# Kernel tuning notes

Hardware: AMD Instinct MI355X
Metric: run time of the kernel (lower is better)

The kernel has to match this reference:

```python
import jax, jax.numpy as jnp
import numpy as np

B, T, D_IN, H, D_OUT = 256, 2048, 128, 128, 128


def setup_inputs() -> dict:
    key = jax.random.key(0)
    ks = jax.random.split(key, 7)
    s_in = 1.0 / np.sqrt(H)
    return {
        "x": jax.random.normal(ks[0], (B, T, D_IN), dtype=jnp.float32),
        "Wih": jax.random.normal(ks[1], (4 * H, D_IN), dtype=jnp.float32) * s_in,
        "Whh": jax.random.normal(ks[2], (4 * H, H), dtype=jnp.float32) * s_in,
        "bih": jax.random.normal(ks[3], (4 * H,), dtype=jnp.float32) * s_in,
        "bhh": jax.random.normal(ks[4], (4 * H,), dtype=jnp.float32) * s_in,
        "Wo": jax.random.normal(ks[5], (D_OUT, H), dtype=jnp.float32) * s_in,
        "bo": jax.random.normal(ks[6], (D_OUT,), dtype=jnp.float32) * s_in,
    }


def reference(x, Wih, Whh, bih, bhh, Wo, bo):
    # LSTM recurrence over time; module returns only the last step's
    # output projection (outputs[:, -1, :]).
    batch, seq_len, _ = x.shape
    h0 = jnp.zeros((batch, Whh.shape[1]), dtype=x.dtype)
    c0 = jnp.zeros_like(h0)
    # Precompute input-side gate projections for all timesteps in one GEMM.
    xg = jnp.einsum('btd,gd->btg', x, Wih) + bih + bhh  # [B, T, 4H]
    xg = jnp.swapaxes(xg, 0, 1)  # [T, B, 4H] for scan

    def step(carry, xg_t):
        h, c = carry
        gates = xg_t + h @ Whh.T  # [B, 4H]
        i, f, g, o = jnp.split(gates, 4, axis=-1)
        i = jax.nn.sigmoid(i)
        f = jax.nn.sigmoid(f)
        g = jnp.tanh(g)
        o = jax.nn.sigmoid(o)
        c = f * c + i * g
        h = o * jnp.tanh(c)
        return (h, c), None

    (h_last, _), _ = jax.lax.scan(step, (h0, c0), xg)
    return h_last @ Wo.T + bo  # [B, D_OUT]
```

## Files before the change

kernel.cpp:

```cpp
#include <hip/hip_runtime.h>
#include <hip/hip_fp16.h>

#define B_  256
#define T_  2048
#define D_  128
#define H_  128
#define CH  32
#define NCH (T_ / CH)
#define XGP (4 * H_ + 8)

#define NLOG2E  (-1.4426950408889634f)
#define LOG2E2  ( 2.8853900817779268f)

typedef __attribute__((ext_vector_type(8))) _Float16 half8v;
typedef __attribute__((ext_vector_type(2))) _Float16 half2v;
typedef __attribute__((ext_vector_type(4))) float    floatx4;

static __device__ __forceinline__ unsigned pkh(float a, float b) {
  return __builtin_bit_cast(unsigned, __builtin_amdgcn_cvt_pkrtz(a, b));
}
static __device__ __forceinline__ float h2f_lo(unsigned u) {
  return __half2float(__ushort_as_half((unsigned short)(u & 0xffffu)));
}
static __device__ __forceinline__ float h2f_hi(unsigned u) {
  return __half2float(__ushort_as_half((unsigned short)(u >> 16)));
}
static __device__ __forceinline__ float fdot2(unsigned h, unsigned w, float c) {
  return __builtin_amdgcn_fdot2(__builtin_bit_cast(half2v, h),
                                __builtin_bit_cast(half2v, w), c, false);
}
template <int CTRL>
static __device__ __forceinline__ float dppadd(float v) {
  int t = __builtin_amdgcn_update_dpp(0, __builtin_bit_cast(int, v),
                                      CTRL, 0xF, 0xF, false);
  return v + __builtin_bit_cast(float, t);
}

__global__ __attribute__((amdgpu_flat_work_group_size(512, 512),
                          amdgpu_waves_per_eu(2, 2)))
void lstm_dot2(
    const float* __restrict__ x,   const float* __restrict__ Wih,
    const float* __restrict__ Whh, const float* __restrict__ bih,
    const float* __restrict__ bhh, const float* __restrict__ Wo,
    const float* __restrict__ bo,  float* __restrict__ out)
{
  __shared__ unsigned       xs[CH][68];
  __shared__ unsigned short xgf[CH][XGP];
  __shared__ __align__(16) unsigned hbuf[2][64];

  const int tid  = threadIdx.x;
  const int b    = blockIdx.x;
  const int lane = tid & 63;
  const int wv   = tid >> 6;
  const int quad = lane >> 4;
  const int m16  = lane & 15;
  const int unit_l = quad * 4 + (m16 & 3);
  const int unit_g = wv * 16 + unit_l;
  const int kq   = m16 >> 2;

  unsigned wd[4][16];
  #pragma unroll
  for (int g = 0; g < 4; ++g) {
    float s = (g == 2) ? LOG2E2 : NLOG2E;
    const float4* p =
        (const float4*)(Whh + (size_t)(g * 128 + unit_g) * H_) + kq * 8;
    #pragma unroll
    for (int q = 0; q < 8; ++q) {
      float4 f = p[q];
      wd[g][q * 2]     = pkh(f.x * s, f.y * s);
      wd[g][q * 2 + 1] = pkh(f.z * s, f.w * s);
    }
  }

  const float sW = ((wv >> 1) == 2) ? LOG2E2 : NLOG2E;
  uint4 wb[4][4];
  float bv[4];
  #pragma unroll
  for (int nt = 0; nt < 4; ++nt) {
    int gcol = wv * 64 + nt * 16 + m16;
    const float4* p = (const float4*)(Wih + (size_t)gcol * D_);
    #pragma unroll
    for (int kf = 0; kf < 4; ++kf) {
      float4 f0 = p[kf * 8 + quad * 2];
      float4 f1 = p[kf * 8 + quad * 2 + 1];
      uint4 u;
      u.x = pkh(f0.x * sW, f0.y * sW);  u.y = pkh(f0.z * sW, f0.w * sW);
      u.z = pkh(f1.x * sW, f1.y * sW);  u.w = pkh(f1.z * sW, f1.w * sW);
      wb[nt][kf] = u;
    }
    bv[nt] = (bih[gcol] + bhh[gcol]) * sW;
  }

  if (tid < 128) hbuf[tid >> 6][tid & 63] = 0u;
  const floatx4 zf = {0.f, 0.f, 0.f, 0.f};
  float c = 0.0f;
  __syncthreads();

  const float* xb = x + (size_t)b * T_ * D_;

  for (int ch = 0; ch < NCH; ++ch) {
    const float4* xsrc = (const float4*)(xb + (size_t)ch * CH * D_);
    #pragma unroll
    for (int i = 0; i < 2; ++i) {
      int fi = i * 512 + tid;
      float4 v = xsrc[fi];
      int t  = fi >> 5;
      int kp = (fi & 31) * 2;
      xs[t][kp]     = pkh(v.x, v.y);
      xs[t][kp + 1] = pkh(v.z, v.w);
    }
    __syncthreads();

    #pragma unroll
    for (int mt = 0; mt < 2; ++mt) {
      half8v af[4];
      #pragma unroll
      for (int kf = 0; kf < 4; ++kf)
        af[kf] = __builtin_bit_cast(half8v,
                   *(const uint4*)&xs[mt * 16 + m16][kf * 16 + quad * 4]);
      #pragma unroll
      for (int nt = 0; nt < 4; ++nt) {
        floatx4 acc = zf;
        #pragma unroll
        for (int kf = 0; kf < 4; ++kf)
          acc = __builtin_amdgcn_mfma_f32_16x16x32_f16(
              af[kf], __builtin_bit_cast(half8v, wb[nt][kf]), acc, 0, 0, 0);
        int gcol = wv * 64 + nt * 16 + m16;
        int jc   = gcol & 127, gt = gcol >> 7;
        #pragma unroll
        for (int r = 0; r < 4; ++r) {
          int trow = mt * 16 + quad * 4 + r;
          xgf[trow][jc * 4 + gt] =
              __half_as_ushort(__float2half((acc[r] + bv[nt]) * 0.25f));
        }
      }
    }
    __syncthreads();

    #pragma unroll 2
    for (int tt = 0; tt < CH; ++tt) {
      const int rp = tt & 1;
      unsigned long long xv =
          *(const unsigned long long*)&xgf[tt][unit_g * 4];
      const unsigned* hb = &hbuf[rp][kq * 16];
      unsigned hs[16];
      *(uint4*)&hs[0]  = *(const uint4*)(hb + 0);
      *(uint4*)&hs[4]  = *(const uint4*)(hb + 4);
      *(uint4*)&hs[8]  = *(const uint4*)(hb + 8);
      *(uint4*)&hs[12] = *(const uint4*)(hb + 12);
      unsigned xlo = (unsigned)xv, xhi = (unsigned)(xv >> 32);
      float ai = h2f_lo(xlo), af_ = h2f_hi(xlo);
      float ag = h2f_lo(xhi), ao  = h2f_hi(xhi);
      #pragma unroll
      for (int p = 0; p < 16; ++p) {
        ai  = fdot2(hs[p], wd[0][p], ai);
        af_ = fdot2(hs[p], wd[1][p], af_);
        ag  = fdot2(hs[p], wd[2][p], ag);
        ao  = fdot2(hs[p], wd[3][p], ao);
      }
      ai  = dppadd<0x124>(dppadd<0x128>(ai));
      af_ = dppadd<0x124>(dppadd<0x128>(af_));
      ag  = dppadd<0x124>(dppadd<0x128>(ag));
      ao  = dppadd<0x124>(dppadd<0x128>(ao));
      float gi = __builtin_amdgcn_rcpf(1.0f + __builtin_amdgcn_exp2f(ai));
      float gf = __builtin_amdgcn_rcpf(1.0f + __builtin_amdgcn_exp2f(af_));
      float go = __builtin_amdgcn_rcpf(1.0f + __builtin_amdgcn_exp2f(ao));
      float gg = 1.0f - 2.0f * __builtin_amdgcn_rcpf(
                     1.0f + __builtin_amdgcn_exp2f(ag));
      c = gf * c + gi * gg;
      float tc = 1.0f - 2.0f * __builtin_amdgcn_rcpf(
                     1.0f + __builtin_amdgcn_exp2f(c * LOG2E2));
      float h = go * tc;
      if (m16 < 4)
        ((unsigned short*)hbuf[rp ^ 1])[unit_g] =
            __half_as_ushort(__float2half(h));
      __syncthreads();
    }
  }

  if (tid < H_) {
    float acc = bo[tid];
    const float4* wr = (const float4*)(Wo + (size_t)tid * H_);
    const uint2* hp = (const uint2*)hbuf[0];
    #pragma unroll
    for (int k4 = 0; k4 < 32; ++k4) {
      float4 w  = wr[k4];
      uint2  hu = hp[k4];
      acc += w.x * h2f_lo(hu.x) + w.y * h2f_hi(hu.x)
           + w.z * h2f_lo(hu.y) + w.w * h2f_hi(hu.y);
    }
    out[(size_t)b * H_ + tid] = acc;
  }
}

extern "C" void kernel_launch(void* const* d_in, const int* in_sizes, int n_in,
                              void* d_out, int out_size, void* d_ws, size_t ws_size,
                              hipStream_t stream) {
  (void)in_sizes; (void)n_in; (void)d_ws; (void)ws_size; (void)out_size;
  const float* x   = (const float*)d_in[0];
  const float* Wih = (const float*)d_in[1];
  const float* Whh = (const float*)d_in[2];
  const float* bih = (const float*)d_in[3];
  const float* bhh = (const float*)d_in[4];
  const float* Wo  = (const float*)d_in[5];
  const float* bo  = (const float*)d_in[6];
  lstm_dot2<<<B_, 512, 0, stream>>>(x, Wih, Whh, bih, bhh, Wo, bo, (float*)d_out);
}
```

Before: 1.413 ms.

## Split recurrent gate matvec between MFMA (i,f) and fdot2 (g,o) paths

The per-timestep h·Whh product for the input and forget gates now runs on MFMA 16x16x32 instructions, with h broadcast as the B operand. The g and o gates keep the VALU fdot2 path with DPP reductions. Splitting the work this way halves the fdot2 chain on the serial critical path and uses the matrix cores in parallel with it. The cost is wasted MFMA columns, extra LDS loads of h per step, and per-lane selection of the accumulator element.

```diff
diff --git a/kernel.cpp b/kernel.cpp
--- a/kernel.cpp
+++ b/kernel.cpp
@@ -35,10 +35,12 @@
                                       CTRL, 0xF, 0xF, false);
   return v + __builtin_bit_cast(float, t);
 }
+#define SEL4(v, n) (((n) & 2) ? (((n) & 1) ? (v)[3] : (v)[2]) \
+                              : (((n) & 1) ? (v)[1] : (v)[0]))
 
 __global__ __attribute__((amdgpu_flat_work_group_size(512, 512),
                           amdgpu_waves_per_eu(2, 2)))
-void lstm_dot2(
+void lstm_hyb(
     const float* __restrict__ x,   const float* __restrict__ Wih,
     const float* __restrict__ Whh, const float* __restrict__ bih,
     const float* __restrict__ bhh, const float* __restrict__ Wo,
@@ -58,17 +60,34 @@
   const int unit_g = wv * 16 + unit_l;
   const int kq   = m16 >> 2;
 
-  unsigned wd[4][16];
+  uint4 wa[2][4];
   #pragma unroll
-  for (int g = 0; g < 4; ++g) {
-    float s = (g == 2) ? LOG2E2 : NLOG2E;
-    const float4* p =
-        (const float4*)(Whh + (size_t)(g * 128 + unit_g) * H_) + kq * 8;
+  for (int g = 0; g < 2; ++g) {
+    const float4* p = (const float4*)(Whh + (size_t)(g * 128 + wv * 16 + m16) * H_);
+    #pragma unroll
+    for (int kf = 0; kf < 4; ++kf) {
+      float4 f0 = p[kf * 8 + quad * 2];
+      float4 f1 = p[kf * 8 + quad * 2 + 1];
+      uint4 u;
+      u.x = pkh(f0.x * NLOG2E, f0.y * NLOG2E);  u.y = pkh(f0.z * NLOG2E, f0.w * NLOG2E);
+      u.z = pkh(f1.x * NLOG2E, f1.y * NLOG2E);  u.w = pkh(f1.z * NLOG2E, f1.w * NLOG2E);
+      wa[g][kf] = u;
+    }
+  }
+
+  unsigned wdg[16], wdo[16];
+  {
+    const float4* pg =
+        (const float4*)(Whh + (size_t)(2 * 128 + unit_g) * H_) + kq * 8;
+    const float4* po =
+        (const float4*)(Whh + (size_t)(3 * 128 + unit_g) * H_) + kq * 8;
     #pragma unroll
     for (int q = 0; q < 8; ++q) {
-      float4 f = p[q];
-      wd[g][q * 2]     = pkh(f.x * s, f.y * s);
-      wd[g][q * 2 + 1] = pkh(f.z * s, f.w * s);
+      float4 fg = pg[q], fo = po[q];
+      wdg[q * 2]     = pkh(fg.x * LOG2E2, fg.y * LOG2E2);
+      wdg[q * 2 + 1] = pkh(fg.z * LOG2E2, fg.w * LOG2E2);
+      wdo[q * 2]     = pkh(fo.x * NLOG2E, fo.y * NLOG2E);
+      wdo[q * 2 + 1] = pkh(fo.z * NLOG2E, fo.w * NLOG2E);
     }
   }
 
@@ -142,28 +161,50 @@
       const int rp = tt & 1;
       unsigned long long xv =
           *(const unsigned long long*)&xgf[tt][unit_g * 4];
+      uint4 hfr[4];
+      #pragma unroll
+      for (int kf = 0; kf < 4; ++kf)
+        hfr[kf] = *(const uint4*)&hbuf[rp][kf * 16 + quad * 4];
       const unsigned* hb = &hbuf[rp][kq * 16];
       unsigned hs[16];
       *(uint4*)&hs[0]  = *(const uint4*)(hb + 0);
       *(uint4*)&hs[4]  = *(const uint4*)(hb + 4);
       *(uint4*)&hs[8]  = *(const uint4*)(hb + 8);
       *(uint4*)&hs[12] = *(const uint4*)(hb + 12);
+
+      floatx4 accI, accF;
+      {
+        half8v hbv = __builtin_bit_cast(half8v, hfr[0]);
+        accI = __builtin_amdgcn_mfma_f32_16x16x32_f16(
+                   __builtin_bit_cast(half8v, wa[0][0]), hbv, zf, 0, 0, 0);
+        accF = __builtin_amdgcn_mfma_f32_16x16x32_f16(
+                   __builtin_bit_cast(half8v, wa[1][0]), hbv, zf, 0, 0, 0);
+      }
+      #pragma unroll
+      for (int kf = 1; kf < 4; ++kf) {
+        half8v hbv = __builtin_bit_cast(half8v, hfr[kf]);
+        accI = __builtin_amdgcn_mfma_f32_16x16x32_f16(
+                   __builtin_bit_cast(half8v, wa[0][kf]), hbv, accI, 0, 0, 0);
+        accF = __builtin_amdgcn_mfma_f32_16x16x32_f16(
+                   __builtin_bit_cast(half8v, wa[1][kf]), hbv, accF, 0, 0, 0);
+      }
+
       unsigned xlo = (unsigned)xv, xhi = (unsigned)(xv >> 32);
-      float ai = h2f_lo(xlo), af_ = h2f_hi(xlo);
-      float ag = h2f_lo(xhi), ao  = h2f_hi(xhi);
+      float ag = h2f_lo(xhi), ao = h2f_hi(xhi);
       #pragma unroll
       for (int p = 0; p < 16; ++p) {
-        ai  = fdot2(hs[p], wd[0][p], ai);
-        af_ = fdot2(hs[p], wd[1][p], af_);
-        ag  = fdot2(hs[p], wd[2][p], ag);
-        ao  = fdot2(hs[p], wd[3][p], ao);
-      }
-      ai  = dppadd<0x124>(dppadd<0x128>(ai));
-      af_ = dppadd<0x124>(dppadd<0x128>(af_));
-      ag  = dppadd<0x124>(dppadd<0x128>(ag));
-      ao  = dppadd<0x124>(dppadd<0x128>(ao));
-      float gi = __builtin_amdgcn_rcpf(1.0f + __builtin_amdgcn_exp2f(ai));
-      float gf = __builtin_amdgcn_rcpf(1.0f + __builtin_amdgcn_exp2f(af_));
+        ag = fdot2(hs[p], wdg[p], ag);
+        ao = fdot2(hs[p], wdo[p], ao);
+      }
+      ag = dppadd<0x124>(dppadd<0x128>(ag));
+      ao = dppadd<0x124>(dppadd<0x128>(ao));
+
+      const int n = m16 & 3;
+      float pi = fmaf(4.0f, h2f_lo(xlo), SEL4(accI, n));
+      float pf = fmaf(4.0f, h2f_hi(xlo), SEL4(accF, n));
+
+      float gi = __builtin_amdgcn_rcpf(1.0f + __builtin_amdgcn_exp2f(pi));
+      float gf = __builtin_amdgcn_rcpf(1.0f + __builtin_amdgcn_exp2f(pf));
       float go = __builtin_amdgcn_rcpf(1.0f + __builtin_amdgcn_exp2f(ao));
       float gg = 1.0f - 2.0f * __builtin_amdgcn_rcpf(
                      1.0f + __builtin_amdgcn_exp2f(ag));
@@ -171,7 +212,7 @@
       float tc = 1.0f - 2.0f * __builtin_amdgcn_rcpf(
                      1.0f + __builtin_amdgcn_exp2f(c * LOG2E2));
       float h = go * tc;
-      if (m16 < 4)
+      if (kq == 0)
         ((unsigned short*)hbuf[rp ^ 1])[unit_g] =
             __half_as_ushort(__float2half(h));
       __syncthreads();
@@ -204,5 +245,5 @@
   const float* bhh = (const float*)d_in[4];
   const float* Wo  = (const float*)d_in[5];
   const float* bo  = (const float*)d_in[6];
-  lstm_dot2<<<B_, 512, 0, stream>>>(x, Wih, Whh, bih, bhh, Wo, bo, (float*)d_out);
-}
+  lstm_hyb<<<B_, 512, 0, stream>>>(x, Wih, Whh, bih, bhh, Wo, bo, (float*)d_out);
+}
```

Result: slower. 1.560 ms (+10.4%).

## Assign one gate row per lane with packed fp16 FMAs and bpermute gate exchange

Applied to the files above, without the earlier changes.

The recurrent step now gives each lane a full 128-wide Whh row for one gate, instead of four gates over a quarter of the hidden dimension. It accumulates the row with packed half2 FMAs into 8 fp16 partial sums, then folds those sums with fdot2 against ones. The four gate activations are gathered across lane quadrants with ds_bpermute instead of a DPP cross-lane reduction, and the xg layout drops the 0.25 pre-scale. The aim is fewer dot-product instructions on the serial per-timestep path. In exchange, fp16 accumulation lowers accuracy, the bpermute round-trips add latency, and register pressure rises.

```diff
diff --git a/kernel.cpp b/kernel.cpp
--- a/kernel.cpp
+++ b/kernel.cpp
@@ -7,7 +7,7 @@
 #define H_  128
 #define CH  32
 #define NCH (T_ / CH)
-#define XGP (4 * H_ + 8)
+#define XGW (4 * H_ + 8)
 
 #define NLOG2E  (-1.4426950408889634f)
 #define LOG2E2  ( 2.8853900817779268f)
@@ -25,50 +25,49 @@
 static __device__ __forceinline__ float h2f_hi(unsigned u) {
   return __half2float(__ushort_as_half((unsigned short)(u >> 16)));
 }
-static __device__ __forceinline__ float fdot2(unsigned h, unsigned w, float c) {
-  return __builtin_amdgcn_fdot2(__builtin_bit_cast(half2v, h),
-                                __builtin_bit_cast(half2v, w), c, false);
-}
-template <int CTRL>
-static __device__ __forceinline__ float dppadd(float v) {
-  int t = __builtin_amdgcn_update_dpp(0, __builtin_bit_cast(int, v),
-                                      CTRL, 0xF, 0xF, false);
-  return v + __builtin_bit_cast(float, t);
+static __device__ __forceinline__ float fdot2u(unsigned a, unsigned b, float c) {
+  return __builtin_amdgcn_fdot2(__builtin_bit_cast(half2v, a),
+                                __builtin_bit_cast(half2v, b), c, false);
+}
+static __device__ __forceinline__ float sel4r(float a, float b, float c, float d,
+                                              int k) {
+  float lo = (k & 1) ? b : a;
+  float hi = (k & 1) ? d : c;
+  return (k & 2) ? hi : lo;
 }
 
 __global__ __attribute__((amdgpu_flat_work_group_size(512, 512),
                           amdgpu_waves_per_eu(2, 2)))
-void lstm_dot2(
+void lstm_pk(
     const float* __restrict__ x,   const float* __restrict__ Wih,
     const float* __restrict__ Whh, const float* __restrict__ bih,
     const float* __restrict__ bhh, const float* __restrict__ Wo,
     const float* __restrict__ bo,  float* __restrict__ out)
 {
   __shared__ unsigned       xs[CH][68];
-  __shared__ unsigned short xgf[CH][XGP];
+  __shared__ unsigned short xgf[CH][XGW];
   __shared__ __align__(16) unsigned hbuf[2][64];
 
   const int tid  = threadIdx.x;
   const int b    = blockIdx.x;
-  const int lane = tid & 63;
+  const int l    = tid & 63;
   const int wv   = tid >> 6;
-  const int quad = lane >> 4;
-  const int m16  = lane & 15;
-  const int unit_l = quad * 4 + (m16 & 3);
-  const int unit_g = wv * 16 + unit_l;
-  const int kq   = m16 >> 2;
-
-  unsigned wd[4][16];
-  #pragma unroll
-  for (int g = 0; g < 4; ++g) {
-    float s = (g == 2) ? LOG2E2 : NLOG2E;
-    const float4* p =
-        (const float4*)(Whh + (size_t)(g * 128 + unit_g) * H_) + kq * 8;
-    #pragma unroll
-    for (int q = 0; q < 8; ++q) {
-      float4 f = p[q];
-      wd[g][q * 2]     = pkh(f.x * s, f.y * s);
-      wd[g][q * 2 + 1] = pkh(f.z * s, f.w * s);
+  const int quad = l >> 4;
+  const int m16  = l & 15;
+  const int t    = l >> 4;
+  const int j    = l & 15;
+  const int u    = wv * 16 + j;
+  const int r    = t * 128 + u;
+
+  const float s = (t == 2) ? LOG2E2 : NLOG2E;
+  unsigned wd[64];
+  {
+    const float4* wp = (const float4*)(Whh + (size_t)r * H_);
+    #pragma unroll
+    for (int q = 0; q < 32; ++q) {
+      float4 f = wp[q];
+      wd[2 * q]     = pkh(f.x * s, f.y * s);
+      wd[2 * q + 1] = pkh(f.z * s, f.w * s);
     }
   }
 
@@ -83,10 +82,10 @@
     for (int kf = 0; kf < 4; ++kf) {
       float4 f0 = p[kf * 8 + quad * 2];
       float4 f1 = p[kf * 8 + quad * 2 + 1];
-      uint4 u;
-      u.x = pkh(f0.x * sW, f0.y * sW);  u.y = pkh(f0.z * sW, f0.w * sW);
-      u.z = pkh(f1.x * sW, f1.y * sW);  u.w = pkh(f1.z * sW, f1.w * sW);
-      wb[nt][kf] = u;
+      uint4 uu;
+      uu.x = pkh(f0.x * sW, f0.y * sW);  uu.y = pkh(f0.z * sW, f0.w * sW);
+      uu.z = pkh(f1.x * sW, f1.y * sW);  uu.w = pkh(f1.z * sW, f1.w * sW);
+      wb[nt][kf] = uu;
     }
     bv[nt] = (bih[gcol] + bhh[gcol]) * sW;
   }
@@ -96,7 +95,9 @@
   float c = 0.0f;
   __syncthreads();
 
-  const float* xb = x + (size_t)b * T_ * D_;
+  const float* xb  = x + (size_t)b * T_ * D_;
+  const int    a16 = (l ^ 16) << 2;
+  const int    a32 = (l ^ 32) << 2;
 
   for (int ch = 0; ch < NCH; ++ch) {
     const float4* xsrc = (const float4*)(xb + (size_t)ch * CH * D_);
@@ -104,10 +105,10 @@
     for (int i = 0; i < 2; ++i) {
       int fi = i * 512 + tid;
       float4 v = xsrc[fi];
-      int t  = fi >> 5;
+      int tt = fi >> 5;
       int kp = (fi & 31) * 2;
-      xs[t][kp]     = pkh(v.x, v.y);
-      xs[t][kp + 1] = pkh(v.z, v.w);
+      xs[tt][kp]     = pkh(v.x, v.y);
+      xs[tt][kp + 1] = pkh(v.z, v.w);
     }
     __syncthreads();
 
@@ -126,12 +127,11 @@
           acc = __builtin_amdgcn_mfma_f32_16x16x32_f16(
               af[kf], __builtin_bit_cast(half8v, wb[nt][kf]), acc, 0, 0, 0);
         int gcol = wv * 64 + nt * 16 + m16;
-        int jc   = gcol & 127, gt = gcol >> 7;
         #pragma unroll
-        for (int r = 0; r < 4; ++r) {
-          int trow = mt * 16 + quad * 4 + r;
-          xgf[trow][jc * 4 + gt] =
-              __half_as_ushort(__float2half((acc[r] + bv[nt]) * 0.25f));
+        for (int rr = 0; rr < 4; ++rr) {
+          int trow = mt * 16 + quad * 4 + rr;
+          xgf[trow][gcol] =
+              __half_as_ushort(__float2half(acc[rr] + bv[nt]));
         }
       }
     }
@@ -140,40 +140,54 @@
     #pragma unroll 2
     for (int tt = 0; tt < CH; ++tt) {
       const int rp = tt & 1;
-      unsigned long long xv =
-          *(const unsigned long long*)&xgf[tt][unit_g * 4];
-      const unsigned* hb = &hbuf[rp][kq * 16];
-      unsigned hs[16];
-      *(uint4*)&hs[0]  = *(const uint4*)(hb + 0);
-      *(uint4*)&hs[4]  = *(const uint4*)(hb + 4);
-      *(uint4*)&hs[8]  = *(const uint4*)(hb + 8);
-      *(uint4*)&hs[12] = *(const uint4*)(hb + 12);
-      unsigned xlo = (unsigned)xv, xhi = (unsigned)(xv >> 32);
-      float ai = h2f_lo(xlo), af_ = h2f_hi(xlo);
-      float ag = h2f_lo(xhi), ao  = h2f_hi(xhi);
-      #pragma unroll
-      for (int p = 0; p < 16; ++p) {
-        ai  = fdot2(hs[p], wd[0][p], ai);
-        af_ = fdot2(hs[p], wd[1][p], af_);
-        ag  = fdot2(hs[p], wd[2][p], ag);
-        ao  = fdot2(hs[p], wd[3][p], ao);
-      }
-      ai  = dppadd<0x124>(dppadd<0x128>(ai));
-      af_ = dppadd<0x124>(dppadd<0x128>(af_));
-      ag  = dppadd<0x124>(dppadd<0x128>(ag));
-      ao  = dppadd<0x124>(dppadd<0x128>(ao));
-      float gi = __builtin_amdgcn_rcpf(1.0f + __builtin_amdgcn_exp2f(ai));
-      float gf = __builtin_amdgcn_rcpf(1.0f + __builtin_amdgcn_exp2f(af_));
-      float go = __builtin_amdgcn_rcpf(1.0f + __builtin_amdgcn_exp2f(ao));
-      float gg = 1.0f - 2.0f * __builtin_amdgcn_rcpf(
-                     1.0f + __builtin_amdgcn_exp2f(ag));
+      unsigned hs[64];
+      const uint4* hb4 = (const uint4*)hbuf[rp];
+      #pragma unroll
+      for (int q = 0; q < 16; ++q)
+        *(uint4*)&hs[4 * q] = hb4[q];
+      float pre0 = __half2float(__ushort_as_half(xgf[tt][r]));
+
+      __half2 acc8[8];
+      #pragma unroll
+      for (int q = 0; q < 8; ++q)
+        acc8[q] = __builtin_bit_cast(__half2, 0u);
+      #pragma unroll
+      for (int p = 0; p < 64; ++p)
+        acc8[p & 7] = __hfma2(__builtin_bit_cast(__half2, hs[p]),
+                              __builtin_bit_cast(__half2, wd[p]),
+                              acc8[p & 7]);
+      const unsigned ONE2 = 0x3C003C00u;
+      float cA = pre0, cB = 0.f;
+      #pragma unroll
+      for (int q = 0; q < 4; ++q)
+        cA = fdot2u(__builtin_bit_cast(unsigned, acc8[q]), ONE2, cA);
+      #pragma unroll
+      for (int q = 4; q < 8; ++q)
+        cB = fdot2u(__builtin_bit_cast(unsigned, acc8[q]), ONE2, cB);
+      float pre = cA + cB;
+
+      float rr  = __builtin_amdgcn_rcpf(1.0f + __builtin_amdgcn_exp2f(pre));
+      float val = (t == 2) ? fmaf(-2.0f, rr, 1.0f) : rr;
+
+      int vb  = __builtin_bit_cast(int, val);
+      int w16 = __builtin_amdgcn_ds_bpermute(a16, vb);
+      int w32 = __builtin_amdgcn_ds_bpermute(a32, vb);
+      int w48 = __builtin_amdgcn_ds_bpermute(a32, w16);
+      float S0 = val;
+      float S1 = __builtin_bit_cast(float, w16);
+      float S2 = __builtin_bit_cast(float, w32);
+      float S3 = __builtin_bit_cast(float, w48);
+      float gi = sel4r(S0, S1, S2, S3, t);
+      float gf = sel4r(S0, S1, S2, S3, t ^ 1);
+      float gg = sel4r(S0, S1, S2, S3, t ^ 2);
+      float go = sel4r(S0, S1, S2, S3, t ^ 3);
+
       c = gf * c + gi * gg;
       float tc = 1.0f - 2.0f * __builtin_amdgcn_rcpf(
                      1.0f + __builtin_amdgcn_exp2f(c * LOG2E2));
       float h = go * tc;
-      if (m16 < 4)
-        ((unsigned short*)hbuf[rp ^ 1])[unit_g] =
-            __half_as_ushort(__float2half(h));
+      if (t == 0)
+        ((unsigned short*)hbuf[rp ^ 1])[u] = __half_as_ushort(__float2half(h));
       __syncthreads();
     }
   }
@@ -204,5 +218,5 @@
   const float* bhh = (const float*)d_in[4];
   const float* Wo  = (const float*)d_in[5];
   const float* bo  = (const float*)d_in[6];
-  lstm_dot2<<<B_, 512, 0, stream>>>(x, Wih, Whh, bih, bhh, Wo, bo, (float*)d_out);
-}
+  lstm_pk<<<B_, 512, 0, stream>>>(x, Wih, Whh, bih, bhh, Wo, bo, (float*)d_out);
+}
```

Result: slower. 1.747 ms (+23.6%).
